# Kernel tuning notes

Hardware: AMD Instinct MI355X
Metric: run time of the kernel (lower is better)

Reference implementation:

```python
import jax, jax.numpy as jnp
import numpy as np

EPS = 1e-5

def spmm(rows, cols, vals, x, n_out):
    # COO sparse [n_out, n_in] @ x [n_in, d] -> [n_out, d]
    return jax.ops.segment_sum(vals[:, None] * x[cols], rows, num_segments=n_out)

def layernorm(x, g, b):
    mu = jnp.mean(x, axis=-1, keepdims=True)
    var = jnp.var(x, axis=-1, keepdims=True)
    return (x - mu) * jax.lax.rsqrt(var + EPS) * g + b

def setup_inputs() -> dict:
    key = jax.random.key(0)
    ks = jax.random.split(key, 32)
    N, D = 100000, 512
    N0, N1, N2 = 131072, 32768, 8192
    E_s0, E_s1 = 262144, 65536
    E_f0, E_f1 = 1048576, 262144
    s = 1.0 / np.sqrt(D)
    inp = {
        'x': jax.random.normal(ks[0], (N, D), jnp.float32),
        'hist0': jax.random.normal(ks[1], (N, D), jnp.float32),
        'hist1': jax.random.normal(ks[2], (N, D), jnp.float32),
        'w0': jax.random.normal(ks[3], (D, D), jnp.float32) * s,
        'b0': jax.random.normal(ks[4], (D,), jnp.float32) * s,
        'g0': jnp.ones((D,), jnp.float32),
        'beta0': jnp.zeros((D,), jnp.float32),
        'w1': jax.random.normal(ks[5], (D, D), jnp.float32) * s,
        'b1': jax.random.normal(ks[6], (D,), jnp.float32) * s,
        'sadj0_vals': jax.random.uniform(ks[7], (E_s0,), jnp.float32),
        'sadj1_vals': jax.random.uniform(ks[8], (E_s1,), jnp.float32),
        'fadj0_vals': jax.random.uniform(ks[9], (E_f0,), jnp.float32),
        'fadj1_vals': jax.random.uniform(ks[10], (E_f1,), jnp.float32),
        'sid0': jax.random.randint(ks[11], (N0,), 0, N),
        'sid1': jax.random.randint(ks[12], (N1,), 0, N),
        'sid2': jax.random.randint(ks[13], (N2,), 0, N),
        'fid0': jax.random.randint(ks[14], (N0,), 0, N),
        'fid1': jax.random.randint(ks[15], (N1,), 0, N),
        'sadj0_rows': jax.random.randint(ks[16], (E_s0,), 0, N1),
        'sadj0_cols': jax.random.randint(ks[17], (E_s0,), 0, N0),
        'sadj1_rows': jax.random.randint(ks[18], (E_s1,), 0, N2),
        'sadj1_cols': jax.random.randint(ks[19], (E_s1,), 0, N1),
        'fadj0_rows': jax.random.randint(ks[20], (E_f0,), 0, N1),
        'fadj0_cols': jax.random.randint(ks[21], (E_f0,), 0, N0),
        'fadj1_rows': jax.random.randint(ks[22], (E_f1,), 0, N2),
        'fadj1_cols': jax.random.randint(ks[23], (E_f1,), 0, N1),
    }
    return inp

def reference(x, hist0, hist1, w0, b0, g0, beta0, w1, b1,
              sadj0_vals, sadj1_vals, fadj0_vals, fadj1_vals,
              sid0, sid1, sid2, fid0, fid1,
              sadj0_rows, sadj0_cols, sadj1_rows, sadj1_cols,
              fadj0_rows, fadj0_cols, fadj1_rows, fadj1_cols):
    N1 = sid1.shape[0]
    N2 = sid2.shape[0]
    sg = jax.lax.stop_gradient
    # layer 0
    h = x[sid0]                                   # [N0, D]
    h = h - sg(hist0[sid0])                        # variance-reduction correction
    full = sg(spmm(fadj0_rows, fadj0_cols, fadj0_vals, hist0[fid0], N1))
    h = spmm(sadj0_rows, sadj0_cols, sadj0_vals, h, N1) + full  # [N1, D]
    h = h @ w0.T + b0
    h = jax.nn.relu(layernorm(h, g0, beta0))
    # layer 1 (last: no norm/relu)
    h = h - sg(hist1[sid1])
    full = sg(spmm(fadj1_rows, fadj1_cols, fadj1_vals, hist1[fid1], N2))
    h = spmm(sadj1_rows, sadj1_cols, sadj1_vals, h, N2) + full  # [N2, D]
    h = h @ w1.T + b1
    return jax.nn.log_softmax(h, axis=-1)
```

## Files before the change

kernel.cpp:

```cpp
#include <hip/hip_runtime.h>

#define D 512
#define NTAB 100000

typedef __bf16 bf16x8 __attribute__((ext_vector_type(8)));
typedef float f32x4 __attribute__((ext_vector_type(4)));
typedef float f32x2 __attribute__((ext_vector_type(2)));

__device__ __forceinline__ unsigned f2bf(float f){
  union { float f; unsigned u; } v; v.f = f;
  unsigned r = v.u + 0x7fffu + ((v.u >> 16) & 1u);
  return r >> 16;
}
__device__ __forceinline__ float bf2f(unsigned h){
  union { unsigned u; float f; } v; v.u = h << 16; return v.f;
}
__device__ __forceinline__ uint2 enc_fp8x8(f32x4 v0, f32x4 v1){
  int lo = __builtin_amdgcn_cvt_pk_fp8_f32(v0[0], v0[1], 0, false);
  lo     = __builtin_amdgcn_cvt_pk_fp8_f32(v0[2], v0[3], lo, true);
  int hi = __builtin_amdgcn_cvt_pk_fp8_f32(v1[0], v1[1], 0, false);
  hi     = __builtin_amdgcn_cvt_pk_fp8_f32(v1[2], v1[3], hi, true);
  return make_uint2((unsigned)lo, (unsigned)hi);
}

#define MA_NS   6400
#define MA_GRID (MA_NS*13 + 512)
#define PER8    (NTAB*D/8)

__global__ __launch_bounds__(256) void k_megaA(
    const int* __restrict__ s0r, int nS0,
    const int* __restrict__ f0r, int nF0, int* __restrict__ cnt0,
    const int* __restrict__ s1r, int nS1, int* __restrict__ cnt_s1,
    const int* __restrict__ f1r, int nF1, int* __restrict__ cnt_f1,
    const float* __restrict__ x, const float* __restrict__ hist0, const float* __restrict__ hist1,
    unsigned char* __restrict__ T0q, unsigned char* __restrict__ H1q,
    const float* __restrict__ w0, const float* __restrict__ w1,
    unsigned short* __restrict__ w0b, unsigned short* __restrict__ w1b)
{
  int b = blockIdx.x, t = threadIdx.x;
  if (b < MA_NS*13){
    int sb = b / 13, r = b % 13;
    if (r == 0){
      int i = sb*256 + t;
      if (i < nS0){ atomicAdd(&cnt0[s0r[i]], 2); return; }
      i -= nS0;
      if (i < nF0){ atomicAdd(&cnt0[f0r[i]], 1); return; }
      i -= nF0;
      if (i < nS1){ atomicAdd(&cnt_s1[s1r[i]], 1); return; }
      i -= nS1;
      atomicAdd(&cnt_f1[f1r[i]], 1);
      return;
    }
    if (r < 9){
      int ci = (sb*8 + (r-1))*256 + t;
      if (ci >= 2*PER8) return;
      const float* src = (ci < PER8) ? x : hist0;
      int ii = (ci < PER8) ? ci : ci - PER8;
      const f32x4* p = (const f32x4*)(src + (size_t)ii*8);
      f32x4 v0 = __builtin_nontemporal_load(p);
      f32x4 v1 = __builtin_nontemporal_load(p+1);
      *(uint2*)(T0q + (size_t)ci*8) = enc_fp8x8(v0, v1);
      return;
    }
    {
      int ci = (sb*4 + (r-9))*256 + t;
      if (ci >= PER8) return;
      const f32x4* p = (const f32x4*)(hist1 + (size_t)ci*8);
      f32x4 v0 = __builtin_nontemporal_load(p);
      f32x4 v1 = __builtin_nontemporal_load(p+1);
      *(uint2*)(H1q + (size_t)ci*8) = enc_fp8x8(v0, v1);
      return;
    }
  } else {
    int i = (b - MA_NS*13)*256 + t;
    const float* src = (i < 65536) ? w0 : w1;
    unsigned short* dst = (i < 65536) ? w0b : w1b;
    int ii = (i < 65536) ? i : i - 65536;
    f32x4 v = *(const f32x4*)(src + (size_t)ii*4);
    ushort4 o;
    o.x = (unsigned short)f2bf(v[0]); o.y = (unsigned short)f2bf(v[1]);
    o.z = (unsigned short)f2bf(v[2]); o.w = (unsigned short)f2bf(v[3]);
    *(ushort4*)(dst + (size_t)ii*4) = o;
  }
}

__global__ __launch_bounds__(1024) void k_exscan3(
    const int* c0, int* r0, int n0,
    const int* c1, int* r1, int n1,
    const int* c2, int* r2, int n2)
{
  __shared__ int part[1024];
  const int* cnt; int* rp; int n;
  switch (blockIdx.x){
    case 0: cnt=c0; rp=r0; n=n0; break;
    case 1: cnt=c1; rp=r1; n=n1; break;
    default: cnt=c2; rp=r2; n=n2; break;
  }
  int t = threadIdx.x;
  int chunk = n >> 10;
  int base = t*chunk;
  int s = 0;
  for (int i=0;i<chunk;i++) s += cnt[base+i];
  part[t] = s; __syncthreads();
  for (int off=1; off<1024; off<<=1){
    int v = (t>=off) ? part[t-off] : 0;
    __syncthreads();
    part[t] += v;
    __syncthreads();
  }
  int run = (t==0) ? 0 : part[t-1];
  for (int i=0;i<chunk;i++){ rp[base+i] = run; run += cnt[base+i]; }
  if (t == 1023) rp[n] = run;
}

__global__ __launch_bounds__(256) void k_fill(
    const int* __restrict__ s0r, const int* __restrict__ s0c, const float* __restrict__ s0v, int nS0,
    const int* __restrict__ f0r, const int* __restrict__ f0c, const float* __restrict__ f0v, int nF0,
    const int* __restrict__ sid0, const int* __restrict__ fid0,
    const int* __restrict__ rp0, int* __restrict__ fill0, int2* __restrict__ bce0,
    const int* __restrict__ s1r, const int* __restrict__ s1c, const float* __restrict__ s1v, int nS1,
    const int* __restrict__ rp_s1, int* __restrict__ fill_s1, int2* __restrict__ bce_s1,
    const int* __restrict__ f1r, const int* __restrict__ f1c, const float* __restrict__ f1v,
    const int* __restrict__ fid1,
    const int* __restrict__ rp_f1, int* __restrict__ fill_f1, int2* __restrict__ bce_f1)
{
  int i = blockIdx.x*256 + threadIdx.x;
  if (i < nS0){
    int rr = s0r[i];
    int c  = sid0[s0c[i]];
    float v = s0v[i];
    int p = atomicAdd(&fill0[rr], 2);
    int base = rp0[rr] + p;
    bce0[base]   = make_int2(c,        __float_as_int(v));
    bce0[base+1] = make_int2(NTAB + c, __float_as_int(-v));
    return;
  }
  i -= nS0;
  if (i < nF0){
    int rr = f0r[i];
    int c  = NTAB + fid0[f0c[i]];
    int p = atomicAdd(&fill0[rr], 1);
    bce0[rp0[rr] + p] = make_int2(c, __float_as_int(f0v[i]));
    return;
  }
  i -= nF0;
  if (i < nS1){
    int rr = s1r[i];
    int p = atomicAdd(&fill_s1[rr], 1);
    bce_s1[rp_s1[rr] + p] = make_int2(s1c[i], __float_as_int(s1v[i]));
    return;
  }
  i -= nS1;
  {
    int rr = f1r[i];
    int c  = fid1[f1c[i]];
    int p = atomicAdd(&fill_f1[rr], 1);
    bce_f1[rp_f1[rr] + p] = make_int2(c, __float_as_int(f1v[i]));
  }
}

__device__ __forceinline__ void acc_bf16(float* a, uint4 p, float v){
  a[0] += v*bf2f(p.x & 0xffffu); a[1] += v*bf2f(p.x >> 16);
  a[2] += v*bf2f(p.y & 0xffffu); a[3] += v*bf2f(p.y >> 16);
  a[4] += v*bf2f(p.z & 0xffffu); a[5] += v*bf2f(p.z >> 16);
  a[6] += v*bf2f(p.w & 0xffffu); a[7] += v*bf2f(p.w >> 16);
}
__device__ __forceinline__ void acc_fp8(float* a, uint2 q, float v){
  f32x2 d0 = __builtin_amdgcn_cvt_pk_f32_fp8(q.x, false);
  f32x2 d1 = __builtin_amdgcn_cvt_pk_f32_fp8(q.x, true);
  f32x2 d2 = __builtin_amdgcn_cvt_pk_f32_fp8(q.y, false);
  f32x2 d3 = __builtin_amdgcn_cvt_pk_f32_fp8(q.y, true);
  a[0] += v*d0[0]; a[1] += v*d0[1]; a[2] += v*d1[0]; a[3] += v*d1[1];
  a[4] += v*d2[0]; a[5] += v*d2[1]; a[6] += v*d3[0]; a[7] += v*d3[1];
}

__device__ __forceinline__ void spmm_phase(
    const int* __restrict__ rp, const int2* __restrict__ be,
    const unsigned short* __restrict__ H, int row, int lane, float* a)
{
  int j = rp[row], je = rp[row+1];
  for (; j + 8 <= je; j += 8){
    int2 e[8]; uint4 p[8];
    #pragma unroll
    for (int u=0;u<8;u++) e[u] = be[j+u];
    #pragma unroll
    for (int u=0;u<8;u++) p[u] = *(const uint4*)(H + (size_t)e[u].x*D + lane*8);
    #pragma unroll
    for (int u=0;u<8;u++) acc_bf16(a, p[u], __int_as_float(e[u].y));
  }
  if (j + 4 <= je){
    int2 e[4]; uint4 p[4];
    #pragma unroll
    for (int u=0;u<4;u++) e[u] = be[j+u];
    #pragma unroll
    for (int u=0;u<4;u++) p[u] = *(const uint4*)(H + (size_t)e[u].x*D + lane*8);
    #pragma unroll
    for (int u=0;u<4;u++) acc_bf16(a, p[u], __int_as_float(e[u].y));
    j += 4;
  }
  for (; j < je; j++){
    int2 e = be[j];
    uint4 p = *(const uint4*)(H + (size_t)e.x*D + lane*8);
    acc_bf16(a, p, __int_as_float(e.y));
  }
}

__device__ __forceinline__ void spmm_phase_q8(
    const int* __restrict__ rp, const int2* __restrict__ be,
    const unsigned char* __restrict__ Q, int row, int lane, float* a)
{
  int j = rp[row], je = rp[row+1];
  for (; j + 8 <= je; j += 8){
    int2 e[8]; uint2 q[8];
    #pragma unroll
    for (int u=0;u<8;u++) e[u] = be[j+u];
    #pragma unroll
    for (int u=0;u<8;u++) q[u] = *(const uint2*)(Q + (size_t)e[u].x*D + lane*8);
    #pragma unroll
    for (int u=0;u<8;u++) acc_fp8(a, q[u], __int_as_float(e[u].y));
  }
  if (j + 4 <= je){
    int2 e[4]; uint2 q[4];
    #pragma unroll
    for (int u=0;u<4;u++) e[u] = be[j+u];
    #pragma unroll
    for (int u=0;u<4;u++) q[u] = *(const uint2*)(Q + (size_t)e[u].x*D + lane*8);
    #pragma unroll
    for (int u=0;u<4;u++) acc_fp8(a, q[u], __int_as_float(e[u].y));
    j += 4;
  }
  for (; j < je; j++){
    int2 e = be[j];
    uint2 q = *(const uint2*)(Q + (size_t)e.x*D + lane*8);
    acc_fp8(a, q, __int_as_float(e.y));
  }
}

__device__ __forceinline__ void store_row(unsigned short* out, int row, int lane, const float* a){
  uint4 o;
  o.x = f2bf(a[0]) | (f2bf(a[1]) << 16);
  o.y = f2bf(a[2]) | (f2bf(a[3]) << 16);
  o.z = f2bf(a[4]) | (f2bf(a[5]) << 16);
  o.w = f2bf(a[6]) | (f2bf(a[7]) << 16);
  *(uint4*)(out + (size_t)row*D + lane*8) = o;
}

__global__ __launch_bounds__(256) void k_spmm0(
    const int* __restrict__ rp, const int2* __restrict__ be,
    const unsigned char* __restrict__ T0q,
    unsigned short* __restrict__ out, int nrows)
{
  int wid = threadIdx.x >> 6, lane = threadIdx.x & 63;
  int row = blockIdx.x*4 + wid;
  if (row >= nrows) return;
  float a[8] = {0.f,0.f,0.f,0.f,0.f,0.f,0.f,0.f};
  spmm_phase_q8(rp, be, T0q, row, lane, a);
  store_row(out, row, lane, a);
}

__global__ __launch_bounds__(256) void k_spmm_acc(
    const int* __restrict__ rp, const int2* __restrict__ be, const unsigned short* __restrict__ H,
    unsigned short* __restrict__ out, int nrows)
{
  int wid = threadIdx.x >> 6, lane = threadIdx.x & 63;
  int row = blockIdx.x*4 + wid;
  if (row >= nrows) return;
  float a[8];
  uint4 p = *(const uint4*)(out + (size_t)row*D + lane*8);
  a[0]=bf2f(p.x&0xffffu); a[1]=bf2f(p.x>>16); a[2]=bf2f(p.y&0xffffu); a[3]=bf2f(p.y>>16);
  a[4]=bf2f(p.z&0xffffu); a[5]=bf2f(p.z>>16); a[6]=bf2f(p.w&0xffffu); a[7]=bf2f(p.w>>16);
  spmm_phase(rp, be, H, row, lane, a);
  store_row(out, row, lane, a);
}

__device__ __forceinline__ void gload16(const unsigned short* g, unsigned short* l){
  __builtin_amdgcn_global_load_lds(
      (const __attribute__((address_space(1))) unsigned int*)(const void*)g,
      (__attribute__((address_space(3))) unsigned int*)(void*)l,
      16, 0, 0);
}

template<bool OUT_BF16>
__device__ __forceinline__ void gemm_block(
    const unsigned short* __restrict__ A,
    const unsigned short* __restrict__ B,
    const float* __restrict__ bias,
    void* __restrict__ Cv,
    int gemm_bid, unsigned short* Al, unsigned short* Bl)
{
  int bx = gemm_bid & 3, by = gemm_bid >> 2;
  int m0 = by << 7, n0 = bx << 7;
  int t = threadIdx.x, wave = t >> 6, lane = t & 63;
  int wr = wave >> 1, wc = wave & 1;
  f32x4 acc[4][4] = {};
  int flat = t << 3;
  int r0 = flat >> 5, cc = flat & 31;
  const unsigned short* pa = A + (size_t)(m0 + r0)*D + cc;
  const unsigned short* pb = B + (size_t)(n0 + r0)*D + cc;
  for (int k0 = 0; k0 < D; k0 += 32){
    gload16(pa + k0,                 &Al[flat]);
    gload16(pa + (size_t)64*D + k0,  &Al[flat + 2048]);
    gload16(pb + k0,                 &Bl[flat]);
    gload16(pb + (size_t)64*D + k0,  &Bl[flat + 2048]);
    __syncthreads();
    int arow = (wr << 6) | (lane & 15);
    int brow = (wc << 6) | (lane & 15);
    int kg   = (lane >> 4) << 3;
    bf16x8 af[4], bfr[4];
    #pragma unroll
    for (int mi=0; mi<4; mi++) af[mi]  = *(const bf16x8*)&Al[(arow + (mi<<4))*32 + kg];
    #pragma unroll
    for (int ni=0; ni<4; ni++) bfr[ni] = *(const bf16x8*)&Bl[(brow + (ni<<4))*32 + kg];
    #pragma unroll
    for (int mi=0; mi<4; mi++)
      #pragma unroll
      for (int ni=0; ni<4; ni++)
        acc[mi][ni] = __builtin_amdgcn_mfma_f32_16x16x32_bf16(af[mi], bfr[ni], acc[mi][ni], 0, 0, 0);
    __syncthreads();
  }
  int crow = m0 + (wr << 6) + ((lane >> 4) << 2);
  int ccol = n0 + (wc << 6) + (lane & 15);
  #pragma unroll
  for (int mi=0; mi<4; mi++){
    #pragma unroll
    for (int q=0; q<4; q++){
      int row = crow + (mi << 4) + q;
      #pragma unroll
      for (int ni=0; ni<4; ni++){
        float val = acc[mi][ni][q] + bias[ccol + (ni << 4)];
        if (OUT_BF16)
          ((unsigned short*)Cv)[(size_t)row*D + ccol + (ni << 4)] = (unsigned short)f2bf(val);
        else
          ((float*)Cv)[(size_t)row*D + ccol + (ni << 4)] = val;
      }
    }
  }
}

__global__ __launch_bounds__(256) void k_megaC(
    const unsigned short* __restrict__ A, const unsigned short* __restrict__ B,
    const float* __restrict__ bias, unsigned short* __restrict__ y1,
    const int* __restrict__ rpf, const int2* __restrict__ bef,
    const unsigned char* __restrict__ H1q, unsigned short* __restrict__ out2, int n2rows)
{
  __shared__ unsigned short Al[128*32];
  __shared__ unsigned short Bl[128*32];
  int b = blockIdx.x, t = threadIdx.x;
  int sb = b / 3, r = b % 3;
  if (r == 0){
    gemm_block<true>(A, B, bias, (void*)y1, sb, Al, Bl);
  } else {
    int wid = t >> 6, lane = t & 63;
    int row = (sb*2 + (r-1))*4 + wid;
    if (row >= n2rows) return;
    float a[8] = {0.f,0.f,0.f,0.f,0.f,0.f,0.f,0.f};
    spmm_phase_q8(rpf, bef, H1q, row, lane, a);
    store_row(out2, row, lane, a);
  }
}

template<bool OUT_BF16>
__global__ __launch_bounds__(256) void k_gemm_bias(
    const unsigned short* __restrict__ A,
    const unsigned short* __restrict__ B,
    const float* __restrict__ bias,
    void* __restrict__ Cv,
    int M)
{
  __shared__ unsigned short Al[128*32];
  __shared__ unsigned short Bl[128*32];
  gemm_block<OUT_BF16>(A, B, bias, Cv, blockIdx.x, Al, Bl);
}

__global__ __launch_bounds__(256) void k_ln_relu_subq(
    const unsigned short* __restrict__ y, const float* __restrict__ gam, const float* __restrict__ bet,
    const unsigned char* __restrict__ H1q, const int* __restrict__ sid1,
    unsigned short* __restrict__ out)
{
  __shared__ float sh[8];
  int row = blockIdx.x, t = threadIdx.x;
  int c = t << 1;
  unsigned pv = *(const unsigned*)(y + (size_t)row*D + c);
  float vx = bf2f(pv & 0xffffu), vy = bf2f(pv >> 16);
  float s = vx + vy, ss = vx*vx + vy*vy;
  #pragma unroll
  for (int m=1; m<64; m<<=1){ s += __shfl_xor(s, m); ss += __shfl_xor(ss, m); }
  int wave = t >> 6, lane = t & 63;
  if (lane == 0){ sh[wave] = s; sh[4+wave] = ss; }
  __syncthreads();
  s  = sh[0]+sh[1]+sh[2]+sh[3];
  ss = sh[4]+sh[5]+sh[6]+sh[7];
  float mu  = s * (1.f/D);
  float var = ss * (1.f/D) - mu*mu;
  float rr  = rsqrtf(var + 1e-5f);
  int srow = sid1[row];
  unsigned short qv = *(const unsigned short*)(H1q + (size_t)srow*D + c);
  f32x2 d = __builtin_amdgcn_cvt_pk_f32_fp8((unsigned)qv, false);
  float o0 = fmaxf((vx - mu)*rr*gam[c]   + bet[c],   0.f) - d[0];
  float o1 = fmaxf((vy - mu)*rr*gam[c+1] + bet[c+1], 0.f) - d[1];
  *(unsigned*)(out + (size_t)row*D + c) = f2bf(o0) | (f2bf(o1) << 16);
}

__global__ __launch_bounds__(256) void k_logsoftmax(const float* __restrict__ y, float* __restrict__ out){
  __shared__ float sh[8];
  int row = blockIdx.x, t = threadIdx.x;
  int c = t << 1;
  float2 v = *(const float2*)(y + (size_t)row*D + c);
  float m = fmaxf(v.x, v.y);
  #pragma unroll
  for (int k=1; k<64; k<<=1) m = fmaxf(m, __shfl_xor(m, k));
  int wave = t >> 6, lane = t & 63;
  if (lane == 0) sh[wave] = m;
  __syncthreads();
  m = fmaxf(fmaxf(sh[0], sh[1]), fmaxf(sh[2], sh[3]));
  __syncthreads();
  float e = expf(v.x - m) + expf(v.y - m);
  #pragma unroll
  for (int k=1; k<64; k<<=1) e += __shfl_xor(e, k);
  if (lane == 0) sh[4+wave] = e;
  __syncthreads();
  e = sh[4]+sh[5]+sh[6]+sh[7];
  float lse = m + logf(e);
  float2 o; o.x = v.x - lse; o.y = v.y - lse;
  *(float2*)(out + (size_t)row*D + c) = o;
}

extern "C" void kernel_launch(void* const* d_in, const int* in_sizes, int n_in,
                              void* d_out, int out_size, void* d_ws, size_t ws_size,
                              hipStream_t stream)
{
  const float* x     = (const float*)d_in[0];
  const float* hist0 = (const float*)d_in[1];
  const float* hist1 = (const float*)d_in[2];
  const float* w0    = (const float*)d_in[3];
  const float* b0    = (const float*)d_in[4];
  const float* g0    = (const float*)d_in[5];
  const float* beta0 = (const float*)d_in[6];
  const float* w1    = (const float*)d_in[7];
  const float* b1    = (const float*)d_in[8];
  const float* s0v   = (const float*)d_in[9];
  const float* s1v   = (const float*)d_in[10];
  const float* f0v   = (const float*)d_in[11];
  const float* f1v   = (const float*)d_in[12];
  const int* sid0    = (const int*)d_in[13];
  const int* sid1    = (const int*)d_in[14];
  const int* fid0    = (const int*)d_in[16];
  const int* fid1    = (const int*)d_in[17];
  const int* s0r     = (const int*)d_in[18];
  const int* s0c     = (const int*)d_in[19];
  const int* s1r     = (const int*)d_in[20];
  const int* s1c     = (const int*)d_in[21];
  const int* f0r     = (const int*)d_in[22];
  const int* f0c     = (const int*)d_in[23];
  const int* f1r     = (const int*)d_in[24];
  const int* f1c     = (const int*)d_in[25];

  const int N1 = 32768, N2 = 8192;
  const int Es0 = 262144, Es1 = 65536, Ef0 = 1048576, Ef1 = 262144;
  const int E0 = 2*Es0 + Ef0;

  char* ws = (char*)d_ws;
  size_t off = 0;
  auto alloc = [&](size_t bytes)->char*{
    char* p = ws + off; off += (bytes + 255) & ~(size_t)255; return p;
  };
  char* T0q_raw = alloc((size_t)2*NTAB*D);
  unsigned char* H1q = (unsigned char*)alloc((size_t)NTAB*D);
  unsigned short* h1   = (unsigned short*)alloc((size_t)N1*D*2);
  unsigned short* out1 = (unsigned short*)alloc((size_t)N1*D*2);
  unsigned short* w0b  = (unsigned short*)alloc((size_t)D*D*2);
  unsigned short* w1b  = (unsigned short*)alloc((size_t)D*D*2);
  int* meta = (int*)alloc((size_t)(2*N1 + 4*N2)*4);
  int* cnt0   = meta;            int* fill0   = cnt0 + N1;
  int* cnt_s1 = fill0 + N1;      int* fill_s1 = cnt_s1 + N2;
  int* cnt_f1 = fill_s1 + N2;    int* fill_f1 = cnt_f1 + N2;
  size_t metaBytes = (size_t)(2*N1 + 4*N2)*4;
  int* rp0   = (int*)alloc((size_t)(N1+1)*4);
  int* rp_s1 = (int*)alloc((size_t)(N2+1)*4);
  int* rp_f1 = (int*)alloc((size_t)(N2+1)*4);
  int2* bce0   = (int2*)alloc((size_t)E0*8);
  int2* bce_s1 = (int2*)alloc((size_t)Es1*8);
  int2* bce_f1 = (int2*)alloc((size_t)Ef1*8);

  unsigned char*  T0q  = (unsigned char*)T0q_raw;
  unsigned short* y1   = (unsigned short*)T0q_raw;
  float*          y2   = (float*)(T0q_raw + ((size_t)34<<20));
  unsigned short* out2 = (unsigned short*)(T0q_raw + ((size_t)52<<20));
  float*          outp = (float*)d_out;

  hipMemsetAsync(meta, 0, metaBytes, stream);
  k_megaA<<<MA_GRID, 256, 0, stream>>>(
      s0r, Es0, f0r, Ef0, cnt0, s1r, Es1, cnt_s1, f1r, Ef1, cnt_f1,
      x, hist0, hist1, T0q, H1q, w0, w1, w0b, w1b);
  k_exscan3<<<3, 1024, 0, stream>>>(cnt0, rp0, N1, cnt_s1, rp_s1, N2, cnt_f1, rp_f1, N2);
  k_fill<<<6400, 256, 0, stream>>>(
      s0r, s0c, s0v, Es0, f0r, f0c, f0v, Ef0, sid0, fid0, rp0, fill0, bce0,
      s1r, s1c, s1v, Es1, rp_s1, fill_s1, bce_s1,
      f1r, f1c, f1v, fid1, rp_f1, fill_f1, bce_f1);
  k_spmm0<<<N1/4, 256, 0, stream>>>(rp0, bce0, T0q, out1, N1);
  k_megaC<<<1024*3, 256, 0, stream>>>(out1, w0b, b0, y1, rp_f1, bce_f1, H1q, out2, N2);
  k_ln_relu_subq<<<N1, 256, 0, stream>>>(y1, g0, beta0, H1q, sid1, h1);
  k_spmm_acc<<<N2/4, 256, 0, stream>>>(rp_s1, bce_s1, h1, out2, N2);
  k_gemm_bias<false><<<(N2/128)*4, 256, 0, stream>>>(out2, w1b, b1, (void*)y2, N2);
  k_logsoftmax<<<N2, 256, 0, stream>>>(y2, outp);
}
```

Before: 528.7 us.

## Move quantization into fill kernel; split counting into its own pass

The edge counting moves into a small standalone kernel. The bucket-fill work is merged with the fp8/bf16 conversion of x, hist0, hist1 and the weights in one large kernel that runs after the exclusive scan. The scatter atomics can then overlap with the streaming conversion instead of the cheap counting pass. The layer-1 LayerNorm now subtracts full-precision hist1 instead of the fp8 copy, which reads more bytes but removes that quantization error.

After: 566.5 us. +7.2%, slower.

```diff
diff --git a/kernel.cpp b/kernel.cpp
--- a/kernel.cpp
+++ b/kernel.cpp
@@ -23,32 +23,108 @@
   return make_uint2((unsigned)lo, (unsigned)hi);
 }
 
-#define MA_NS   6400
-#define MA_GRID (MA_NS*13 + 512)
-#define PER8    (NTAB*D/8)
-
-__global__ __launch_bounds__(256) void k_megaA(
-    const int* __restrict__ s0r, int nS0,
-    const int* __restrict__ f0r, int nF0, int* __restrict__ cnt0,
+#define PER8 (NTAB*D/8)
+
+__global__ __launch_bounds__(256) void k_count(
+    const int* __restrict__ s0r, int nS0, int* __restrict__ cnt0,
+    const int* __restrict__ f0r, int nF0,
     const int* __restrict__ s1r, int nS1, int* __restrict__ cnt_s1,
-    const int* __restrict__ f1r, int nF1, int* __restrict__ cnt_f1,
+    const int* __restrict__ f1r, int nF1, int* __restrict__ cnt_f1)
+{
+  int i = blockIdx.x*256 + threadIdx.x;
+  if (i < nS0){ atomicAdd(&cnt0[s0r[i]], 2); return; }
+  i -= nS0;
+  if (i < nF0){ atomicAdd(&cnt0[f0r[i]], 1); return; }
+  i -= nF0;
+  if (i < nS1){ atomicAdd(&cnt_s1[s1r[i]], 1); return; }
+  i -= nS1;
+  atomicAdd(&cnt_f1[f1r[i]], 1);
+}
+
+__global__ __launch_bounds__(1024) void k_exscan3(
+    const int* c0, int* r0, int n0,
+    const int* c1, int* r1, int n1,
+    const int* c2, int* r2, int n2)
+{
+  __shared__ int part[1024];
+  const int* cnt; int* rp; int n;
+  switch (blockIdx.x){
+    case 0: cnt=c0; rp=r0; n=n0; break;
+    case 1: cnt=c1; rp=r1; n=n1; break;
+    default: cnt=c2; rp=r2; n=n2; break;
+  }
+  int t = threadIdx.x;
+  int chunk = n >> 10;
+  int base = t*chunk;
+  int s = 0;
+  for (int i=0;i<chunk;i++) s += cnt[base+i];
+  part[t] = s; __syncthreads();
+  for (int off=1; off<1024; off<<=1){
+    int v = (t>=off) ? part[t-off] : 0;
+    __syncthreads();
+    part[t] += v;
+    __syncthreads();
+  }
+  int run = (t==0) ? 0 : part[t-1];
+  for (int i=0;i<chunk;i++){ rp[base+i] = run; run += cnt[base+i]; }
+  if (t == 1023) rp[n] = run;
+}
+
+#define MF_NS   6400
+#define MF_GRID (MF_NS*13 + 512)
+
+__global__ __launch_bounds__(256) void k_megaF(
+    const int* __restrict__ s0r, const int* __restrict__ s0c, const float* __restrict__ s0v, int nS0,
+    const int* __restrict__ f0r, const int* __restrict__ f0c, const float* __restrict__ f0v, int nF0,
+    const int* __restrict__ sid0, const int* __restrict__ fid0,
+    const int* __restrict__ rp0, int* __restrict__ fill0, int2* __restrict__ bce0,
+    const int* __restrict__ s1r, const int* __restrict__ s1c, const float* __restrict__ s1v, int nS1,
+    const int* __restrict__ rp_s1, int* __restrict__ fill_s1, int2* __restrict__ bce_s1,
+    const int* __restrict__ f1r, const int* __restrict__ f1c, const float* __restrict__ f1v,
+    const int* __restrict__ fid1,
+    const int* __restrict__ rp_f1, int* __restrict__ fill_f1, int2* __restrict__ bce_f1,
     const float* __restrict__ x, const float* __restrict__ hist0, const float* __restrict__ hist1,
     unsigned char* __restrict__ T0q, unsigned char* __restrict__ H1q,
     const float* __restrict__ w0, const float* __restrict__ w1,
     unsigned short* __restrict__ w0b, unsigned short* __restrict__ w1b)
 {
   int b = blockIdx.x, t = threadIdx.x;
-  if (b < MA_NS*13){
+  if (b < MF_NS*13){
     int sb = b / 13, r = b % 13;
     if (r == 0){
       int i = sb*256 + t;
-      if (i < nS0){ atomicAdd(&cnt0[s0r[i]], 2); return; }
+      if (i < nS0){
+        int rr = s0r[i];
+        int c  = sid0[s0c[i]];
+        float v = s0v[i];
+        int p = atomicAdd(&fill0[rr], 2);
+        int base = rp0[rr] + p;
+        bce0[base]   = make_int2(c,        __float_as_int(v));
+        bce0[base+1] = make_int2(NTAB + c, __float_as_int(-v));
+        return;
+      }
       i -= nS0;
-      if (i < nF0){ atomicAdd(&cnt0[f0r[i]], 1); return; }
+      if (i < nF0){
+        int rr = f0r[i];
+        int c  = NTAB + fid0[f0c[i]];
+        int p = atomicAdd(&fill0[rr], 1);
+        bce0[rp0[rr] + p] = make_int2(c, __float_as_int(f0v[i]));
+        return;
+      }
       i -= nF0;
-      if (i < nS1){ atomicAdd(&cnt_s1[s1r[i]], 1); return; }
+      if (i < nS1){
+        int rr = s1r[i];
+        int p = atomicAdd(&fill_s1[rr], 1);
+        bce_s1[rp_s1[rr] + p] = make_int2(s1c[i], __float_as_int(s1v[i]));
+        return;
+      }
       i -= nS1;
-      atomicAdd(&cnt_f1[f1r[i]], 1);
+      {
+        int rr = f1r[i];
+        int c  = fid1[f1c[i]];
+        int p = atomicAdd(&fill_f1[rr], 1);
+        bce_f1[rp_f1[rr] + p] = make_int2(c, __float_as_int(f1v[i]));
+      }
       return;
     }
     if (r < 9){
@@ -72,7 +148,7 @@
       return;
     }
   } else {
-    int i = (b - MA_NS*13)*256 + t;
+    int i = (b - MF_NS*13)*256 + t;
     const float* src = (i < 65536) ? w0 : w1;
     unsigned short* dst = (i < 65536) ? w0b : w1b;
     int ii = (i < 65536) ? i : i - 65536;
@@ -81,81 +157,6 @@
     o.x = (unsigned short)f2bf(v[0]); o.y = (unsigned short)f2bf(v[1]);
     o.z = (unsigned short)f2bf(v[2]); o.w = (unsigned short)f2bf(v[3]);
     *(ushort4*)(dst + (size_t)ii*4) = o;
-  }
-}
-
-__global__ __launch_bounds__(1024) void k_exscan3(
-    const int* c0, int* r0, int n0,
-    const int* c1, int* r1, int n1,
-    const int* c2, int* r2, int n2)
-{
-  __shared__ int part[1024];
-  const int* cnt; int* rp; int n;
-  switch (blockIdx.x){
-    case 0: cnt=c0; rp=r0; n=n0; break;
-    case 1: cnt=c1; rp=r1; n=n1; break;
-    default: cnt=c2; rp=r2; n=n2; break;
-  }
-  int t = threadIdx.x;
-  int chunk = n >> 10;
-  int base = t*chunk;
-  int s = 0;
-  for (int i=0;i<chunk;i++) s += cnt[base+i];
-  part[t] = s; __syncthreads();
-  for (int off=1; off<1024; off<<=1){
-    int v = (t>=off) ? part[t-off] : 0;
-    __syncthreads();
-    part[t] += v;
-    __syncthreads();
-  }
-  int run = (t==0) ? 0 : part[t-1];
-  for (int i=0;i<chunk;i++){ rp[base+i] = run; run += cnt[base+i]; }
-  if (t == 1023) rp[n] = run;
-}
-
-__global__ __launch_bounds__(256) void k_fill(
-    const int* __restrict__ s0r, const int* __restrict__ s0c, const float* __restrict__ s0v, int nS0,
-    const int* __restrict__ f0r, const int* __restrict__ f0c, const float* __restrict__ f0v, int nF0,
-    const int* __restrict__ sid0, const int* __restrict__ fid0,
-    const int* __restrict__ rp0, int* __restrict__ fill0, int2* __restrict__ bce0,
-    const int* __restrict__ s1r, const int* __restrict__ s1c, const float* __restrict__ s1v, int nS1,
-    const int* __restrict__ rp_s1, int* __restrict__ fill_s1, int2* __restrict__ bce_s1,
-    const int* __restrict__ f1r, const int* __restrict__ f1c, const float* __restrict__ f1v,
-    const int* __restrict__ fid1,
-    const int* __restrict__ rp_f1, int* __restrict__ fill_f1, int2* __restrict__ bce_f1)
-{
-  int i = blockIdx.x*256 + threadIdx.x;
-  if (i < nS0){
-    int rr = s0r[i];
-    int c  = sid0[s0c[i]];
-    float v = s0v[i];
-    int p = atomicAdd(&fill0[rr], 2);
-    int base = rp0[rr] + p;
-    bce0[base]   = make_int2(c,        __float_as_int(v));
-    bce0[base+1] = make_int2(NTAB + c, __float_as_int(-v));
-    return;
-  }
-  i -= nS0;
-  if (i < nF0){
-    int rr = f0r[i];
-    int c  = NTAB + fid0[f0c[i]];
-    int p = atomicAdd(&fill0[rr], 1);
-    bce0[rp0[rr] + p] = make_int2(c, __float_as_int(f0v[i]));
-    return;
-  }
-  i -= nF0;
-  if (i < nS1){
-    int rr = s1r[i];
-    int p = atomicAdd(&fill_s1[rr], 1);
-    bce_s1[rp_s1[rr] + p] = make_int2(s1c[i], __float_as_int(s1v[i]));
-    return;
-  }
-  i -= nS1;
-  {
-    int rr = f1r[i];
-    int c  = fid1[f1c[i]];
-    int p = atomicAdd(&fill_f1[rr], 1);
-    bce_f1[rp_f1[rr] + p] = make_int2(c, __float_as_int(f1v[i]));
   }
 }
 
@@ -372,9 +373,9 @@
   gemm_block<OUT_BF16>(A, B, bias, Cv, blockIdx.x, Al, Bl);
 }
 
-__global__ __launch_bounds__(256) void k_ln_relu_subq(
+__global__ __launch_bounds__(256) void k_ln_relu_sub(
     const unsigned short* __restrict__ y, const float* __restrict__ gam, const float* __restrict__ bet,
-    const unsigned char* __restrict__ H1q, const int* __restrict__ sid1,
+    const float* __restrict__ hist1, const int* __restrict__ sid1,
     unsigned short* __restrict__ out)
 {
   __shared__ float sh[8];
@@ -394,10 +395,9 @@
   float var = ss * (1.f/D) - mu*mu;
   float rr  = rsqrtf(var + 1e-5f);
   int srow = sid1[row];
-  unsigned short qv = *(const unsigned short*)(H1q + (size_t)srow*D + c);
-  f32x2 d = __builtin_amdgcn_cvt_pk_f32_fp8((unsigned)qv, false);
-  float o0 = fmaxf((vx - mu)*rr*gam[c]   + bet[c],   0.f) - d[0];
-  float o1 = fmaxf((vy - mu)*rr*gam[c+1] + bet[c+1], 0.f) - d[1];
+  float2 hv = *(const float2*)(hist1 + (size_t)srow*D + c);
+  float o0 = fmaxf((vx - mu)*rr*gam[c]   + bet[c],   0.f) - hv.x;
+  float o1 = fmaxf((vy - mu)*rr*gam[c+1] + bet[c+1], 0.f) - hv.y;
   *(unsigned*)(out + (size_t)row*D + c) = f2bf(o0) | (f2bf(o1) << 16);
 }
 
@@ -489,17 +489,16 @@
   float*          outp = (float*)d_out;
 
   hipMemsetAsync(meta, 0, metaBytes, stream);
-  k_megaA<<<MA_GRID, 256, 0, stream>>>(
-      s0r, Es0, f0r, Ef0, cnt0, s1r, Es1, cnt_s1, f1r, Ef1, cnt_f1,
-      x, hist0, hist1, T0q, H1q, w0, w1, w0b, w1b);
+  k_count<<<6400, 256, 0, stream>>>(s0r, Es0, cnt0, f0r, Ef0, s1r, Es1, cnt_s1, f1r, Ef1, cnt_f1);
   k_exscan3<<<3, 1024, 0, stream>>>(cnt0, rp0, N1, cnt_s1, rp_s1, N2, cnt_f1, rp_f1, N2);
-  k_fill<<<6400, 256, 0, stream>>>(
+  k_megaF<<<MF_GRID, 256, 0, stream>>>(
       s0r, s0c, s0v, Es0, f0r, f0c, f0v, Ef0, sid0, fid0, rp0, fill0, bce0,
       s1r, s1c, s1v, Es1, rp_s1, fill_s1, bce_s1,
-      f1r, f1c, f1v, fid1, rp_f1, fill_f1, bce_f1);
+      f1r, f1c, f1v, fid1, rp_f1, fill_f1, bce_f1,
+      x, hist0, hist1, T0q, H1q, w0, w1, w0b, w1b);
   k_spmm0<<<N1/4, 256, 0, stream>>>(rp0, bce0, T0q, out1, N1);
   k_megaC<<<1024*3, 256, 0, stream>>>(out1, w0b, b0, y1, rp_f1, bce_f1, H1q, out2, N2);
-  k_ln_relu_subq<<<N1, 256, 0, stream>>>(y1, g0, beta0, H1q, sid1, h1);
+  k_ln_relu_sub<<<N1, 256, 0, stream>>>(y1, g0, beta0, hist1, sid1, h1);
   k_spmm_acc<<<N2/4, 256, 0, stream>>>(rp_s1, bce_s1, h1, out2, N2);
   k_gemm_bias<false><<<(N2/128)*4, 256, 0, stream>>>(out2, w1b, b1, (void*)y2, N2);
   k_logsoftmax<<<N2, 256, 0, stream>>>(y2, outp);
```

## Precompute x-hist0 difference table, halve sampled edges, store hist1 as bf16

Applied to the files above, without the earlier changes.

The conversion kernel now encodes (x - hist0) into the first fp8 table instead of encoding x and hist0 separately. Each sampled layer-0 edge therefore needs one gather instead of two (+v and -v). The hist1 table changes from fp8 to bf16, which doubles its conversion write traffic and the gather bytes in the layer-1 full spmm and the LN subtraction. This trades fewer edges and atomics in fill and spmm0 for more bytes on the layer-1 path, in exchange for better accuracy.

After: 526.6 us. Within noise of the previous version (-0.4%).

```diff
diff --git a/kernel.cpp b/kernel.cpp
--- a/kernel.cpp
+++ b/kernel.cpp
@@ -23,9 +23,10 @@
   return make_uint2((unsigned)lo, (unsigned)hi);
 }
 
+#define PER8 (NTAB*D/8)
+
 #define MA_NS   6400
-#define MA_GRID (MA_NS*13 + 512)
-#define PER8    (NTAB*D/8)
+#define MA_GRID (MA_NS*9 + 512)
 
 __global__ __launch_bounds__(256) void k_megaA(
     const int* __restrict__ s0r, int nS0,
@@ -33,16 +34,17 @@
     const int* __restrict__ s1r, int nS1, int* __restrict__ cnt_s1,
     const int* __restrict__ f1r, int nF1, int* __restrict__ cnt_f1,
     const float* __restrict__ x, const float* __restrict__ hist0, const float* __restrict__ hist1,
-    unsigned char* __restrict__ T0q, unsigned char* __restrict__ H1q,
+    unsigned char* __restrict__ TD,
+    unsigned short* __restrict__ H1b,
     const float* __restrict__ w0, const float* __restrict__ w1,
     unsigned short* __restrict__ w0b, unsigned short* __restrict__ w1b)
 {
   int b = blockIdx.x, t = threadIdx.x;
-  if (b < MA_NS*13){
-    int sb = b / 13, r = b % 13;
+  if (b < MA_NS*9){
+    int sb = b / 9, r = b % 9;
     if (r == 0){
       int i = sb*256 + t;
-      if (i < nS0){ atomicAdd(&cnt0[s0r[i]], 2); return; }
+      if (i < nS0){ atomicAdd(&cnt0[s0r[i]], 1); return; }
       i -= nS0;
       if (i < nF0){ atomicAdd(&cnt0[f0r[i]], 1); return; }
       i -= nF0;
@@ -51,28 +53,35 @@
       atomicAdd(&cnt_f1[f1r[i]], 1);
       return;
     }
-    if (r < 9){
-      int ci = (sb*8 + (r-1))*256 + t;
-      if (ci >= 2*PER8) return;
-      const float* src = (ci < PER8) ? x : hist0;
-      int ii = (ci < PER8) ? ci : ci - PER8;
-      const f32x4* p = (const f32x4*)(src + (size_t)ii*8);
-      f32x4 v0 = __builtin_nontemporal_load(p);
-      f32x4 v1 = __builtin_nontemporal_load(p+1);
-      *(uint2*)(T0q + (size_t)ci*8) = enc_fp8x8(v0, v1);
+    if (r < 5){
+      int ci = (sb*4 + (r-1))*256 + t;
+      if (ci >= PER8) return;
+      const f32x4* px = (const f32x4*)(x     + (size_t)ci*8);
+      const f32x4* ph = (const f32x4*)(hist0 + (size_t)ci*8);
+      f32x4 x0 = __builtin_nontemporal_load(px);
+      f32x4 x1 = __builtin_nontemporal_load(px+1);
+      f32x4 h0 = __builtin_nontemporal_load(ph);
+      f32x4 h1 = __builtin_nontemporal_load(ph+1);
+      *(uint2*)(TD + (size_t)ci*8)                    = enc_fp8x8(x0 - h0, x1 - h1);
+      *(uint2*)(TD + (size_t)NTAB*D + (size_t)ci*8)   = enc_fp8x8(h0, h1);
       return;
     }
     {
-      int ci = (sb*4 + (r-9))*256 + t;
+      int ci = (sb*4 + (r-5))*256 + t;
       if (ci >= PER8) return;
       const f32x4* p = (const f32x4*)(hist1 + (size_t)ci*8);
       f32x4 v0 = __builtin_nontemporal_load(p);
       f32x4 v1 = __builtin_nontemporal_load(p+1);
-      *(uint2*)(H1q + (size_t)ci*8) = enc_fp8x8(v0, v1);
+      uint4 o;
+      o.x = f2bf(v0[0]) | (f2bf(v0[1])<<16);
+      o.y = f2bf(v0[2]) | (f2bf(v0[3])<<16);
+      o.z = f2bf(v1[0]) | (f2bf(v1[1])<<16);
+      o.w = f2bf(v1[2]) | (f2bf(v1[3])<<16);
+      *(uint4*)(H1b + (size_t)ci*8) = o;
       return;
     }
   } else {
-    int i = (b - MA_NS*13)*256 + t;
+    int i = (b - MA_NS*9)*256 + t;
     const float* src = (i < 65536) ? w0 : w1;
     unsigned short* dst = (i < 65536) ? w0b : w1b;
     int ii = (i < 65536) ? i : i - 65536;
@@ -128,11 +137,8 @@
   if (i < nS0){
     int rr = s0r[i];
     int c  = sid0[s0c[i]];
-    float v = s0v[i];
-    int p = atomicAdd(&fill0[rr], 2);
-    int base = rp0[rr] + p;
-    bce0[base]   = make_int2(c,        __float_as_int(v));
-    bce0[base+1] = make_int2(NTAB + c, __float_as_int(-v));
+    int p = atomicAdd(&fill0[rr], 1);
+    bce0[rp0[rr] + p] = make_int2(c, __float_as_int(s0v[i]));
     return;
   }
   i -= nS0;
@@ -247,14 +253,14 @@
 
 __global__ __launch_bounds__(256) void k_spmm0(
     const int* __restrict__ rp, const int2* __restrict__ be,
-    const unsigned char* __restrict__ T0q,
+    const unsigned char* __restrict__ TD,
     unsigned short* __restrict__ out, int nrows)
 {
   int wid = threadIdx.x >> 6, lane = threadIdx.x & 63;
   int row = blockIdx.x*4 + wid;
   if (row >= nrows) return;
   float a[8] = {0.f,0.f,0.f,0.f,0.f,0.f,0.f,0.f};
-  spmm_phase_q8(rp, be, T0q, row, lane, a);
+  spmm_phase_q8(rp, be, TD, row, lane, a);
   store_row(out, row, lane, a);
 }
 
@@ -341,7 +347,7 @@
     const unsigned short* __restrict__ A, const unsigned short* __restrict__ B,
     const float* __restrict__ bias, unsigned short* __restrict__ y1,
     const int* __restrict__ rpf, const int2* __restrict__ bef,
-    const unsigned char* __restrict__ H1q, unsigned short* __restrict__ out2, int n2rows)
+    const unsigned short* __restrict__ H1b, unsigned short* __restrict__ out2, int n2rows)
 {
   __shared__ unsigned short Al[128*32];
   __shared__ unsigned short Bl[128*32];
@@ -354,7 +360,7 @@
     int row = (sb*2 + (r-1))*4 + wid;
     if (row >= n2rows) return;
     float a[8] = {0.f,0.f,0.f,0.f,0.f,0.f,0.f,0.f};
-    spmm_phase_q8(rpf, bef, H1q, row, lane, a);
+    spmm_phase(rpf, bef, H1b, row, lane, a);
     store_row(out2, row, lane, a);
   }
 }
@@ -372,9 +378,9 @@
   gemm_block<OUT_BF16>(A, B, bias, Cv, blockIdx.x, Al, Bl);
 }
 
-__global__ __launch_bounds__(256) void k_ln_relu_subq(
+__global__ __launch_bounds__(256) void k_ln_relu_sub(
     const unsigned short* __restrict__ y, const float* __restrict__ gam, const float* __restrict__ bet,
-    const unsigned char* __restrict__ H1q, const int* __restrict__ sid1,
+    const unsigned short* __restrict__ H1b, const int* __restrict__ sid1,
     unsigned short* __restrict__ out)
 {
   __shared__ float sh[8];
@@ -394,10 +400,9 @@
   float var = ss * (1.f/D) - mu*mu;
   float rr  = rsqrtf(var + 1e-5f);
   int srow = sid1[row];
-  unsigned short qv = *(const unsigned short*)(H1q + (size_t)srow*D + c);
-  f32x2 d = __builtin_amdgcn_cvt_pk_f32_fp8((unsigned)qv, false);
-  float o0 = fmaxf((vx - mu)*rr*gam[c]   + bet[c],   0.f) - d[0];
-  float o1 = fmaxf((vy - mu)*rr*gam[c+1] + bet[c+1], 0.f) - d[1];
+  unsigned hv = *(const unsigned*)(H1b + (size_t)srow*D + c);
+  float o0 = fmaxf((vx - mu)*rr*gam[c]   + bet[c],   0.f) - bf2f(hv & 0xffffu);
+  float o1 = fmaxf((vy - mu)*rr*gam[c+1] + bet[c+1], 0.f) - bf2f(hv >> 16);
   *(unsigned*)(out + (size_t)row*D + c) = f2bf(o0) | (f2bf(o1) << 16);
 }
 
@@ -457,15 +462,15 @@
 
   const int N1 = 32768, N2 = 8192;
   const int Es0 = 262144, Es1 = 65536, Ef0 = 1048576, Ef1 = 262144;
-  const int E0 = 2*Es0 + Ef0;
+  const int E0 = Es0 + Ef0;
 
   char* ws = (char*)d_ws;
   size_t off = 0;
   auto alloc = [&](size_t bytes)->char*{
     char* p = ws + off; off += (bytes + 255) & ~(size_t)255; return p;
   };
-  char* T0q_raw = alloc((size_t)2*NTAB*D);
-  unsigned char* H1q = (unsigned char*)alloc((size_t)NTAB*D);
+  char* TD_raw = alloc((size_t)2*NTAB*D);
+  unsigned short* H1b = (unsigned short*)alloc((size_t)NTAB*D*2);
   unsigned short* h1   = (unsigned short*)alloc((size_t)N1*D*2);
   unsigned short* out1 = (unsigned short*)alloc((size_t)N1*D*2);
   unsigned short* w0b  = (unsigned short*)alloc((size_t)D*D*2);
@@ -482,24 +487,24 @@
   int2* bce_s1 = (int2*)alloc((size_t)Es1*8);
   int2* bce_f1 = (int2*)alloc((size_t)Ef1*8);
 
-  unsigned char*  T0q  = (unsigned char*)T0q_raw;
-  unsigned short* y1   = (unsigned short*)T0q_raw;
-  float*          y2   = (float*)(T0q_raw + ((size_t)34<<20));
-  unsigned short* out2 = (unsigned short*)(T0q_raw + ((size_t)52<<20));
+  unsigned char*  TD   = (unsigned char*)TD_raw;
+  unsigned short* y1   = (unsigned short*)TD_raw;
+  float*          y2   = (float*)(TD_raw + ((size_t)34<<20));
+  unsigned short* out2 = (unsigned short*)(TD_raw + ((size_t)52<<20));
   float*          outp = (float*)d_out;
 
   hipMemsetAsync(meta, 0, metaBytes, stream);
   k_megaA<<<MA_GRID, 256, 0, stream>>>(
       s0r, Es0, f0r, Ef0, cnt0, s1r, Es1, cnt_s1, f1r, Ef1, cnt_f1,
-      x, hist0, hist1, T0q, H1q, w0, w1, w0b, w1b);
+      x, hist0, hist1, TD, H1b, w0, w1, w0b, w1b);
   k_exscan3<<<3, 1024, 0, stream>>>(cnt0, rp0, N1, cnt_s1, rp_s1, N2, cnt_f1, rp_f1, N2);
   k_fill<<<6400, 256, 0, stream>>>(
       s0r, s0c, s0v, Es0, f0r, f0c, f0v, Ef0, sid0, fid0, rp0, fill0, bce0,
       s1r, s1c, s1v, Es1, rp_s1, fill_s1, bce_s1,
       f1r, f1c, f1v, fid1, rp_f1, fill_f1, bce_f1);
-  k_spmm0<<<N1/4, 256, 0, stream>>>(rp0, bce0, T0q, out1, N1);
-  k_megaC<<<1024*3, 256, 0, stream>>>(out1, w0b, b0, y1, rp_f1, bce_f1, H1q, out2, N2);
-  k_ln_relu_subq<<<N1, 256, 0, stream>>>(y1, g0, beta0, H1q, sid1, h1);
+  k_spmm0<<<N1/4, 256, 0, stream>>>(rp0, bce0, TD, out1, N1);
+  k_megaC<<<1024*3, 256, 0, stream>>>(out1, w0b, b0, y1, rp_f1, bce_f1, H1b, out2, N2);
+  k_ln_relu_sub<<<N1, 256, 0, stream>>>(y1, g0, beta0, H1b, sid1, h1);
   k_spmm_acc<<<N2/4, 256, 0, stream>>>(rp_s1, bce_s1, h1, out2, N2);
   k_gemm_bias<false><<<(N2/128)*4, 256, 0, stream>>>(out2, w1b, b1, (void*)y2, N2);
   k_logsoftmax<<<N2, 256, 0, stream>>>(y2, outp);
```
